# Kernel tuning notes

Hardware: AMD Instinct MI355X
Metric: run time of the kernel (lower is better)

## Reference

```python
import jax, jax.numpy as jnp
from jax import lax
import numpy as np

B, T, C = 2048, 512, 32  # batch, max_seq_len, num_tags


def setup_inputs() -> dict:
    key = jax.random.key(0)
    k1, k2, k3, k4 = jax.random.split(key, 4)
    logits = jax.random.normal(k1, (B, T, C), dtype=jnp.float32)
    sequence_length = jax.random.randint(k2, (B,), 1, T + 1, dtype=jnp.int32)
    labels = jax.random.randint(k3, (B, T), 0, C, dtype=jnp.int32)
    # learned CRF transition matrix (orthogonal init approximated by normal)
    transitions = jax.random.normal(k4, (C, C), dtype=jnp.float32)
    return dict(logits=logits, sequence_length=sequence_length,
                labels=labels, transitions=transitions)


def _viterbi_decode(logits, transitions, seq_len):
    """tfa_text.crf_decode: returns highest-scoring tag sequence [B, T] int32."""
    Bn, Tn, Cn = logits.shape
    identity_bp = jnp.arange(Cn, dtype=jnp.int32)[None, :]  # carries tag through padding

    def fwd(state, xs):  # state: [B, C] viterbi scores
        logit_t, t = xs
        scores = state[:, :, None] + transitions[None]       # [B, C_prev, C_cur]
        cand = logit_t + jnp.max(scores, axis=1)             # [B, C]
        bp = jnp.argmax(scores, axis=1).astype(jnp.int32)    # [B, C] best prev tag
        active = (t < seq_len)[:, None]
        return (jnp.where(active, cand, state),
                jnp.where(active, bp, identity_bp))

    xs = (jnp.swapaxes(logits[:, 1:], 0, 1), jnp.arange(1, Tn))
    final_state, bps = lax.scan(fwd, logits[:, 0], xs)       # bps: [T-1, B, C]
    last_tag = jnp.argmax(final_state, axis=-1).astype(jnp.int32)  # [B]

    def back(tag, bp):  # tag at t+1 -> tag at t
        prev = jnp.take_along_axis(bp, tag[:, None], axis=1)[:, 0]
        return prev, tag

    first_tag, later_tags = lax.scan(back, last_tag, bps, reverse=True)
    tags = jnp.concatenate([first_tag[None], later_tags], axis=0).T  # [B, T]
    valid = jnp.arange(Tn)[None, :] < seq_len[:, None]
    return jnp.where(valid, tags, 0)


def _crf_log_likelihood(logits, labels, transitions, seq_len):
    """tfa_text.crf_log_likelihood: per-example log-likelihood [B]."""
    Bn, Tn, Cn = logits.shape

    # --- log partition via forward algorithm ---
    def fwd(alpha, xs):
        logit_t, t = xs
        new = jax.nn.logsumexp(alpha[:, :, None] + transitions[None], axis=1) + logit_t
        active = (t < seq_len)[:, None]
        return jnp.where(active, new, alpha), None

    xs = (jnp.swapaxes(logits[:, 1:], 0, 1), jnp.arange(1, Tn))
    alpha, _ = lax.scan(fwd, logits[:, 0], xs)
    log_norm = jax.nn.logsumexp(alpha, axis=-1)  # [B]

    # --- score of gold label sequence ---
    pos = jnp.arange(Tn)
    mask = (pos[None, :] < seq_len[:, None]).astype(logits.dtype)          # [B, T]
    unary = jnp.sum(
        jnp.take_along_axis(logits, labels[..., None], axis=2)[..., 0] * mask,
        axis=1)
    pair_mask = (pos[None, :-1] < (seq_len - 1)[:, None]).astype(logits.dtype)
    binary = jnp.sum(transitions[labels[:, :-1], labels[:, 1:]] * pair_mask, axis=1)

    return unary + binary - log_norm


def reference(logits, sequence_length, labels, transitions):
    # training=True path: labels clamped to >= 0 (already non-negative here)
    labels = jnp.maximum(labels, 0)
    decode_tags = _viterbi_decode(logits, transitions, sequence_length)
    log_likelihood = _crf_log_likelihood(logits, labels, transitions, sequence_length)
    loss = jnp.mean(-log_likelihood)  # recorded via add_loss in the original
    return decode_tags, loss
```

## Files before the change

kernel.cpp:

```cpp
#include <hip/hip_runtime.h>
#include <math.h>

#define BB 2048
#define TT 512
#define CC 32

#if __has_builtin(__builtin_amdgcn_exp2f)
#define EXP2F __builtin_amdgcn_exp2f
#else
#define EXP2F exp2f
#endif
#if __has_builtin(__builtin_amdgcn_logf)
#define LOG2F __builtin_amdgcn_logf
#else
#define LOG2F log2f
#endif

#define LOG2E 1.4426950408889634f
#define LN2   0.6931471805599453f

__global__ void zero_loss_kernel(float* __restrict__ out) {
  if (threadIdx.x == 0) out[(size_t)BB * TT] = 0.0f;
}

__global__ void schedule_kernel(const int* __restrict__ seqlen,
                                int* __restrict__ perm,
                                float* __restrict__ out) {
  __shared__ int s[TT];
  __shared__ int off[TT];
  const int tid = threadIdx.x;
  if (tid == 0) out[(size_t)BB * TT] = 0.0f;
  s[tid] = 0;
  __syncthreads();
  for (int b = tid; b < BB; b += TT) atomicAdd(&s[seqlen[b] - 1], 1);
  __syncthreads();
  for (int d = 1; d < TT; d <<= 1) {
    int v = s[tid] + ((tid + d < TT) ? s[tid + d] : 0);
    __syncthreads();
    s[tid] = v;
    __syncthreads();
  }
  off[tid] = (tid + 1 < TT) ? s[tid + 1] : 0;
  __syncthreads();
  for (int b = tid; b < BB; b += TT) {
    int pos = atomicAdd(&off[seqlen[b] - 1], 1);
    perm[pos] = b;
  }
}

#define ROR(dst, src, K)                                                     \
  dst = __int_as_float(__builtin_amdgcn_update_dpp(                          \
      0, __float_as_int(src), 0x120 | (K), 0xF, 0xF, false));

__device__ __forceinline__ float xor16f(float x, int lane) {
#if __has_builtin(__builtin_amdgcn_permlane16_swap)
  auto r = __builtin_amdgcn_permlane16_swap(__float_as_uint(x),
                                            __float_as_uint(x), false, false);
  return __uint_as_float((lane & 16) ? r[0] : r[1]);
#else
  return __int_as_float(
      __builtin_amdgcn_ds_swizzle(__float_as_int(x), 0x401F));
#endif
}
__device__ __forceinline__ float xor32f(float x, int lane) {
#if __has_builtin(__builtin_amdgcn_permlane32_swap)
  auto r = __builtin_amdgcn_permlane32_swap(__float_as_uint(x),
                                            __float_as_uint(x), false, false);
  return __uint_as_float((lane & 32) ? r[0] : r[1]);
#else
  return __shfl_xor(x, 32);
#endif
}
__device__ __forceinline__ int xor32i(int x, int lane) {
#if __has_builtin(__builtin_amdgcn_permlane32_swap)
  auto r = __builtin_amdgcn_permlane32_swap((unsigned)x, (unsigned)x,
                                            false, false);
  return (int)((lane & 32) ? r[0] : r[1]);
#else
  return __shfl_xor(x, 32);
#endif
}

__global__ __launch_bounds__(128, 2) void crf_kernel(
    const float* __restrict__ logits,
    const int*   __restrict__ seqlen,
    const int*   __restrict__ labels,
    const float* __restrict__ trans,
    float*       __restrict__ out,
    const int*   __restrict__ perm)
{
  __shared__ __align__(16) unsigned char bp_s[(TT - 1) * CC];
  __shared__ __align__(16) unsigned gp_s[(TT / 4) * CC];
  __shared__ unsigned char tag_s[TT];

  const int lane = threadIdx.x & 63;
  const int wv   = threadIdx.x >> 6;
  const int k    = blockIdx.x;

  const int bs0 = perm ? perm[k] : k;
  const int bs1 = perm ? perm[BB - 1 - k] : -1;

  const int i  = lane & 15;
  const int c  = lane & 31;
  const int r  = (lane >> 4) & 1;
  const int pr = (lane < 32) ? r : 1 - r;

  if (wv == 0) {
    float tr2[16];
    int   pidx[16];
#pragma unroll
    for (int kk = 0; kk < 16; ++kk) {
      int p = pr * 16 + ((i - kk) & 15);
      pidx[kk] = p;
      tr2[kk] = trans[p * CC + c];
    }

    for (int sq = 0; sq < 2; ++sq) {
      const int b = sq ? bs1 : bs0;
      if (b < 0) break;
      const int len = seqlen[b];
      const float* lg = logits + (size_t)b * TT * CC;
      const size_t bT = (size_t)b * TT;
      const float* lgc = lg + c;

      float av = lg[c];

      auto vstep = [&](int t, float logit_c) -> int {
        float base = (lane < 32) ? av : xor16f(av, lane);
        float S[16];
        float x;
        S[0] = base + tr2[0];
        ROR(x, base, 1);  S[1]  = x + tr2[1];
        ROR(x, base, 2);  S[2]  = x + tr2[2];
        ROR(x, base, 3);  S[3]  = x + tr2[3];
        ROR(x, base, 4);  S[4]  = x + tr2[4];
        ROR(x, base, 5);  S[5]  = x + tr2[5];
        ROR(x, base, 6);  S[6]  = x + tr2[6];
        ROR(x, base, 7);  S[7]  = x + tr2[7];
        ROR(x, base, 8);  S[8]  = x + tr2[8];
        ROR(x, base, 9);  S[9]  = x + tr2[9];
        ROR(x, base, 10); S[10] = x + tr2[10];
        ROR(x, base, 11); S[11] = x + tr2[11];
        ROR(x, base, 12); S[12] = x + tr2[12];
        ROR(x, base, 13); S[13] = x + tr2[13];
        ROR(x, base, 14); S[14] = x + tr2[14];
        ROR(x, base, 15); S[15] = x + tr2[15];

        float a = fmaxf(fmaxf(S[0], S[1]), S[2]);
        float bq = fmaxf(fmaxf(S[3], S[4]), S[5]);
        float cq = fmaxf(fmaxf(S[6], S[7]), S[8]);
        float dq = fmaxf(fmaxf(S[9], S[10]), S[11]);
        float eq = fmaxf(fmaxf(S[12], S[13]), S[14]);
        float best = fmaxf(fmaxf(fmaxf(a, bq), fmaxf(cq, dq)),
                           fmaxf(eq, S[15]));

        int t8[16];
#pragma unroll
        for (int kk = 0; kk < 16; ++kk)
          t8[kk] = (S[kk] == best) ? pidx[kk] : 63;
        int ma = min(min(t8[0], t8[1]), t8[2]);
        int mb = min(min(t8[3], t8[4]), t8[5]);
        int mc = min(min(t8[6], t8[7]), t8[8]);
        int md = min(min(t8[9], t8[10]), t8[11]);
        int me = min(min(t8[12], t8[13]), t8[14]);
        int bi = min(min(min(ma, mb), min(mc, md)), min(me, t8[15]));

        float ov = xor32f(best, lane);
        int   oi = xor32i(bi, lane);
        bool take = (ov > best) || (ov == best && oi < bi);
        best = take ? ov : best;
        int bpi = take ? oi : bi;
        av = logit_c + best;

        if (lane < 32) bp_s[(t - 1) * CC + c] = (unsigned char)bpi;
        return bpi;
      };

      float Abk[8], Bbk[8];
      auto loadB = [&](float (&bk)[8], int t0) {
#pragma unroll
        for (int s = 0; s < 8; ++s) {
          int tt = t0 + s; tt = tt < len ? tt : len - 1;
          bk[s] = lgc[tt * CC];
        }
      };
      auto runB = [&](float (&bk)[8], int t0) {
        int h1 = 0, h2 = 0, h3 = 0;
#pragma unroll
        for (int s = 0; s < 8; ++s) {
          int tt = t0 + s;
          if (tt < len) {
            int bpi = vstep(tt, bk[s]);
            if ((tt & 3) == 0) {
              int m2 = __builtin_amdgcn_ds_bpermute(bpi << 2, h1);
              int m3 = __builtin_amdgcn_ds_bpermute(m2 << 2, h2);
              int m4 = __builtin_amdgcn_ds_bpermute(m3 << 2, h3);
              unsigned packed = (unsigned)bpi | ((unsigned)m2 << 8) |
                                ((unsigned)m3 << 16) | ((unsigned)m4 << 24);
              if (lane < 32) gp_s[((tt >> 2) - 1) * CC + c] = packed;
            }
            h3 = h2; h2 = h1; h1 = bpi;
          }
        }
      };
      loadB(Abk, 1);
      for (int t0 = 1; t0 < len; t0 += 16) {
        loadB(Bbk, t0 + 8);
        runB(Abk, t0);
        if (t0 + 8 < len) {
          loadB(Abk, t0 + 16);
          runB(Bbk, t0 + 8);
        }
      }

      float v = av; int idx = c;
#pragma unroll
      for (int d = 1; d < 32; d <<= 1) {
        float v2 = __shfl_xor(v, d, 32);
        int   i2 = __shfl_xor(idx, d, 32);
        if (v2 > v || (v2 == v && i2 < idx)) { v = v2; idx = i2; }
      }

      if (lane == 0) {
        int tag = idx;
        int t = len - 1;
        tag_s[t] = (unsigned char)tag;
        while (t > 0 && (t & 3) != 0) {
          tag = bp_s[(t - 1) * CC + tag];
          --t;
          tag_s[t] = (unsigned char)tag;
        }
        while (t >= 4) {
          unsigned u = gp_s[((t >> 2) - 1) * CC + tag];
          tag_s[t - 1] = (unsigned char)(u & 255);
          tag_s[t - 2] = (unsigned char)((u >> 8) & 255);
          tag_s[t - 3] = (unsigned char)((u >> 16) & 255);
          tag = (int)(u >> 24);
          tag_s[t - 4] = (unsigned char)tag;
          t -= 4;
        }
      }

#pragma unroll
      for (int j = 0; j < 8; ++j) {
        int tt = lane + 64 * j;
        float val = (tt < len) ? (float)tag_s[tt] : 0.0f;
        out[bT + tt] = val;
      }
    }

  } else {
    float E[16];
#pragma unroll
    for (int kk = 0; kk < 16; ++kk) {
      int p = pr * 16 + ((i - kk) & 15);
      E[kk] = EXP2F(trans[p * CC + c] * LOG2E);
    }

    float loss_acc = 0.0f;

    for (int sq = 0; sq < 2; ++sq) {
      const int b = sq ? bs1 : bs0;
      if (b < 0) break;
      const int len = seqlen[b];
      const float* lg = logits + (size_t)b * TT * CC;
      const int* lab = labels + (size_t)b * TT;
      const float* lgc = lg + c;

      float P   = EXP2F(lg[c] * LOG2E);
      float Acc = 0.0f;

      auto fstep = [&](float raw_logit) {
        float el = EXP2F(raw_logit * LOG2E);
        float base = (lane < 32) ? P : xor16f(P, lane);
        float x;
        float a0 = base * E[0];
        ROR(x, base, 1);  float a1 = x * E[1];
        ROR(x, base, 2);  float a2 = x * E[2];
        ROR(x, base, 3);  float a3 = x * E[3];
        ROR(x, base, 4);  a0 = fmaf(x, E[4],  a0);
        ROR(x, base, 5);  a1 = fmaf(x, E[5],  a1);
        ROR(x, base, 6);  a2 = fmaf(x, E[6],  a2);
        ROR(x, base, 7);  a3 = fmaf(x, E[7],  a3);
        ROR(x, base, 8);  a0 = fmaf(x, E[8],  a0);
        ROR(x, base, 9);  a1 = fmaf(x, E[9],  a1);
        ROR(x, base, 10); a2 = fmaf(x, E[10], a2);
        ROR(x, base, 11); a3 = fmaf(x, E[11], a3);
        ROR(x, base, 12); a0 = fmaf(x, E[12], a0);
        ROR(x, base, 13); a1 = fmaf(x, E[13], a1);
        ROR(x, base, 14); a2 = fmaf(x, E[14], a2);
        ROR(x, base, 15); a3 = fmaf(x, E[15], a3);
        float part = (a0 + a1) + (a2 + a3);
        float oth  = xor32f(part, lane);
        P = el * (part + oth);
      };

      auto renorm = [&]() {
        float m = P, y;
        ROR(y, m, 8); m = fmaxf(m, y);
        ROR(y, m, 4); m = fmaxf(m, y);
        ROR(y, m, 2); m = fmaxf(m, y);
        ROR(y, m, 1); m = fmaxf(m, y);
        m = fmaxf(m, xor16f(m, lane));
        int e = (int)(__float_as_uint(m) >> 23) - 127;
        P = ldexpf(P, -e);
        Acc += (float)e;
      };

      float Abk[8], Bbk[8];
      auto loadB = [&](float (&bk)[8], int t0) {
#pragma unroll
        for (int s = 0; s < 8; ++s) {
          int tt = t0 + s; tt = tt < len ? tt : len - 1;
          bk[s] = lgc[tt * CC];
        }
      };
      auto runB = [&](float (&bk)[8], int t0) {
#pragma unroll
        for (int s = 0; s < 8; ++s) {
          int tt = t0 + s;
          if (tt < len) {
            fstep(bk[s]);
            if ((tt & 3) == 0) renorm();
          }
        }
      };
      loadB(Abk, 1);
      for (int t0 = 1; t0 < len; t0 += 16) {
        loadB(Bbk, t0 + 8);
        runB(Abk, t0);
        if (t0 + 8 < len) {
          loadB(Abk, t0 + 16);
          runB(Bbk, t0 + 8);
        }
      }

      float uacc = 0.0f, bacc = 0.0f;
#pragma unroll
      for (int j = 0; j < 8; ++j) {
        int tt = lane + 64 * j;
        if (tt < len) {
          int lt = lab[tt];
          uacc += lg[tt * CC + lt];
          if (tt + 1 < len) {
            int ln = lab[tt + 1];
            bacc += trans[lt * CC + ln];
          }
        }
      }
#pragma unroll
      for (int d = 32; d >= 1; d >>= 1) {
        uacc += __shfl_xor(uacc, d);
        bacc += __shfl_xor(bacc, d);
      }

      float ss = P, y2;
      ROR(y2, ss, 8); ss += y2;
      ROR(y2, ss, 4); ss += y2;
      ROR(y2, ss, 2); ss += y2;
      ROR(y2, ss, 1); ss += y2;
      ss += xor16f(ss, lane);
      float log_norm = LN2 * (Acc + LOG2F(ss));

      loss_acc += (uacc + bacc - log_norm);
    }

    if (lane == 0) {
      atomicAdd(out + (size_t)BB * TT, loss_acc * (-1.0f / BB));
    }
  }
}

extern "C" void kernel_launch(void* const* d_in, const int* in_sizes, int n_in,
                              void* d_out, int out_size, void* d_ws, size_t ws_size,
                              hipStream_t stream) {
  const float* logits = (const float*)d_in[0];
  const int*   seqlen = (const int*)d_in[1];
  const int*   labels = (const int*)d_in[2];
  const float* trans  = (const float*)d_in[3];
  float* out = (float*)d_out;

  if (d_ws != nullptr && ws_size >= BB * sizeof(int)) {
    int* perm = (int*)d_ws;
    schedule_kernel<<<1, TT, 0, stream>>>(seqlen, perm, out);
    crf_kernel<<<dim3(BB / 2), dim3(128), 0, stream>>>(
        logits, seqlen, labels, trans, out, perm);
  } else {
    zero_loss_kernel<<<1, 64, 0, stream>>>(out);
    crf_kernel<<<dim3(BB), dim3(128), 0, stream>>>(
        logits, seqlen, labels, trans, out, nullptr);
  }
}
```

Measured before the change: 377.3 us.

## Process one sequence per block with interleaved length schedule and shrunk backpointer buffer

Each block now handles a single sequence instead of pairing a short and a long one, so the grid doubles to BB blocks. The schedule permutation is interleaved so blocks of similar length spread across CUs. The per-step backpointer shared buffer shrinks to a 4-step ring, which raises the occupancy hint to 4 blocks per CU. The loop is split into an unguarded full-chunk path and a guarded tail, and the max exchange is moved ahead of the argmax to shorten the critical path. The cost is losing the length balancing that pairing gave each block, plus relying on the scheduler for load balance.

```diff
diff --git a/kernel.cpp b/kernel.cpp
--- a/kernel.cpp
+++ b/kernel.cpp
@@ -43,8 +43,9 @@
   off[tid] = (tid + 1 < TT) ? s[tid + 1] : 0;
   __syncthreads();
   for (int b = tid; b < BB; b += TT) {
-    int pos = atomicAdd(&off[seqlen[b] - 1], 1);
-    perm[pos] = b;
+    int r = atomicAdd(&off[seqlen[b] - 1], 1);
+    int p = (r & 7) * 256 + (r >> 3);
+    perm[p] = b;
   }
 }
 
@@ -81,7 +82,7 @@
 #endif
 }
 
-__global__ __launch_bounds__(128, 2) void crf_kernel(
+__global__ __launch_bounds__(128, 4) void crf_kernel(
     const float* __restrict__ logits,
     const int*   __restrict__ seqlen,
     const int*   __restrict__ labels,
@@ -89,16 +90,18 @@
     float*       __restrict__ out,
     const int*   __restrict__ perm)
 {
-  __shared__ __align__(16) unsigned char bp_s[(TT - 1) * CC];
+  __shared__ __align__(16) unsigned char bp_s[4 * CC];
   __shared__ __align__(16) unsigned gp_s[(TT / 4) * CC];
   __shared__ unsigned char tag_s[TT];
 
   const int lane = threadIdx.x & 63;
   const int wv   = threadIdx.x >> 6;
-  const int k    = blockIdx.x;
-
-  const int bs0 = perm ? perm[k] : k;
-  const int bs1 = perm ? perm[BB - 1 - k] : -1;
+  const int b    = perm ? perm[blockIdx.x] : blockIdx.x;
+
+  const int len = seqlen[b];
+  const float* lg = logits + (size_t)b * TT * CC;
+  const size_t bT = (size_t)b * TT;
+  const float* lgc = lg + (lane & 31);
 
   const int i  = lane & 15;
   const int c  = lane & 31;
@@ -115,141 +118,152 @@
       tr2[kk] = trans[p * CC + c];
     }
 
-    for (int sq = 0; sq < 2; ++sq) {
-      const int b = sq ? bs1 : bs0;
-      if (b < 0) break;
-      const int len = seqlen[b];
-      const float* lg = logits + (size_t)b * TT * CC;
-      const size_t bT = (size_t)b * TT;
-      const float* lgc = lg + c;
-
-      float av = lg[c];
-
-      auto vstep = [&](int t, float logit_c) -> int {
-        float base = (lane < 32) ? av : xor16f(av, lane);
-        float S[16];
-        float x;
-        S[0] = base + tr2[0];
-        ROR(x, base, 1);  S[1]  = x + tr2[1];
-        ROR(x, base, 2);  S[2]  = x + tr2[2];
-        ROR(x, base, 3);  S[3]  = x + tr2[3];
-        ROR(x, base, 4);  S[4]  = x + tr2[4];
-        ROR(x, base, 5);  S[5]  = x + tr2[5];
-        ROR(x, base, 6);  S[6]  = x + tr2[6];
-        ROR(x, base, 7);  S[7]  = x + tr2[7];
-        ROR(x, base, 8);  S[8]  = x + tr2[8];
-        ROR(x, base, 9);  S[9]  = x + tr2[9];
-        ROR(x, base, 10); S[10] = x + tr2[10];
-        ROR(x, base, 11); S[11] = x + tr2[11];
-        ROR(x, base, 12); S[12] = x + tr2[12];
-        ROR(x, base, 13); S[13] = x + tr2[13];
-        ROR(x, base, 14); S[14] = x + tr2[14];
-        ROR(x, base, 15); S[15] = x + tr2[15];
-
-        float a = fmaxf(fmaxf(S[0], S[1]), S[2]);
-        float bq = fmaxf(fmaxf(S[3], S[4]), S[5]);
-        float cq = fmaxf(fmaxf(S[6], S[7]), S[8]);
-        float dq = fmaxf(fmaxf(S[9], S[10]), S[11]);
-        float eq = fmaxf(fmaxf(S[12], S[13]), S[14]);
-        float best = fmaxf(fmaxf(fmaxf(a, bq), fmaxf(cq, dq)),
-                           fmaxf(eq, S[15]));
-
-        int t8[16];
-#pragma unroll
-        for (int kk = 0; kk < 16; ++kk)
-          t8[kk] = (S[kk] == best) ? pidx[kk] : 63;
-        int ma = min(min(t8[0], t8[1]), t8[2]);
-        int mb = min(min(t8[3], t8[4]), t8[5]);
-        int mc = min(min(t8[6], t8[7]), t8[8]);
-        int md = min(min(t8[9], t8[10]), t8[11]);
-        int me = min(min(t8[12], t8[13]), t8[14]);
-        int bi = min(min(min(ma, mb), min(mc, md)), min(me, t8[15]));
-
-        float ov = xor32f(best, lane);
-        int   oi = xor32i(bi, lane);
-        bool take = (ov > best) || (ov == best && oi < bi);
-        best = take ? ov : best;
-        int bpi = take ? oi : bi;
-        av = logit_c + best;
-
-        if (lane < 32) bp_s[(t - 1) * CC + c] = (unsigned char)bpi;
-        return bpi;
-      };
-
-      float Abk[8], Bbk[8];
-      auto loadB = [&](float (&bk)[8], int t0) {
-#pragma unroll
-        for (int s = 0; s < 8; ++s) {
-          int tt = t0 + s; tt = tt < len ? tt : len - 1;
-          bk[s] = lgc[tt * CC];
+    float av = lg[c];
+
+    auto vstep = [&](int t, float logit_c) -> int {
+      float base = (lane < 32) ? av : xor16f(av, lane);
+      float S[16];
+      float x;
+      S[0] = base + tr2[0];
+      ROR(x, base, 1);  S[1]  = x + tr2[1];
+      ROR(x, base, 2);  S[2]  = x + tr2[2];
+      ROR(x, base, 3);  S[3]  = x + tr2[3];
+      ROR(x, base, 4);  S[4]  = x + tr2[4];
+      ROR(x, base, 5);  S[5]  = x + tr2[5];
+      ROR(x, base, 6);  S[6]  = x + tr2[6];
+      ROR(x, base, 7);  S[7]  = x + tr2[7];
+      ROR(x, base, 8);  S[8]  = x + tr2[8];
+      ROR(x, base, 9);  S[9]  = x + tr2[9];
+      ROR(x, base, 10); S[10] = x + tr2[10];
+      ROR(x, base, 11); S[11] = x + tr2[11];
+      ROR(x, base, 12); S[12] = x + tr2[12];
+      ROR(x, base, 13); S[13] = x + tr2[13];
+      ROR(x, base, 14); S[14] = x + tr2[14];
+      ROR(x, base, 15); S[15] = x + tr2[15];
+
+      float a = fmaxf(fmaxf(S[0], S[1]), S[2]);
+      float bq = fmaxf(fmaxf(S[3], S[4]), S[5]);
+      float cq = fmaxf(fmaxf(S[6], S[7]), S[8]);
+      float dq = fmaxf(fmaxf(S[9], S[10]), S[11]);
+      float eq = fmaxf(fmaxf(S[12], S[13]), S[14]);
+      float best = fmaxf(fmaxf(fmaxf(a, bq), fmaxf(cq, dq)),
+                         fmaxf(eq, S[15]));
+
+      float ov = xor32f(best, lane);
+      av = logit_c + fmaxf(best, ov);
+
+      int t8[16];
+#pragma unroll
+      for (int kk = 0; kk < 16; ++kk)
+        t8[kk] = (S[kk] == best) ? pidx[kk] : 63;
+      int ma = min(min(t8[0], t8[1]), t8[2]);
+      int mb = min(min(t8[3], t8[4]), t8[5]);
+      int mc = min(min(t8[6], t8[7]), t8[8]);
+      int md = min(min(t8[9], t8[10]), t8[11]);
+      int me = min(min(t8[12], t8[13]), t8[14]);
+      int bi = min(min(min(ma, mb), min(mc, md)), min(me, t8[15]));
+
+      int oi = xor32i(bi, lane);
+      bool take = (ov > best) || (ov == best && oi < bi);
+      int bpi = take ? oi : bi;
+
+      bp_s[((t - 1) & 3) * CC + c] = (unsigned char)bpi;
+      return bpi;
+    };
+
+    auto compose = [&](int tt, int b3, int b2, int b1, int b0) {
+      int m2 = __builtin_amdgcn_ds_bpermute(b3 << 2, b2);
+      int m3 = __builtin_amdgcn_ds_bpermute(m2 << 2, b1);
+      int m4 = __builtin_amdgcn_ds_bpermute(m3 << 2, b0);
+      unsigned packed = (unsigned)b3 | ((unsigned)m2 << 8) |
+                        ((unsigned)m3 << 16) | ((unsigned)m4 << 24);
+      gp_s[((tt >> 2) - 1) * CC + c] = packed;
+    };
+
+    float Abk[8], Bbk[8];
+    auto loadC = [&](float (&bk)[8], int t0) {
+#pragma unroll
+      for (int s = 0; s < 8; ++s) {
+        int tt = t0 + s; tt = tt < len ? tt : len - 1;
+        bk[s] = lgc[tt * CC];
+      }
+    };
+    auto runFull = [&](float (&bk)[8], int t0) {
+      int b0 = vstep(t0 + 0, bk[0]);
+      int b1 = vstep(t0 + 1, bk[1]);
+      int b2 = vstep(t0 + 2, bk[2]);
+      int b3 = vstep(t0 + 3, bk[3]);
+      compose(t0 + 3, b3, b2, b1, b0);
+      int b4 = vstep(t0 + 4, bk[4]);
+      int b5 = vstep(t0 + 5, bk[5]);
+      int b6 = vstep(t0 + 6, bk[6]);
+      int b7 = vstep(t0 + 7, bk[7]);
+      compose(t0 + 7, b7, b6, b5, b4);
+    };
+    auto runGuard = [&](float (&bk)[8], int t0) {
+      int h1 = 0, h2 = 0, h3 = 0;
+#pragma unroll
+      for (int s = 0; s < 8; ++s) {
+        int tt = t0 + s;
+        if (tt < len) {
+          int bpi = vstep(tt, bk[s]);
+          if ((tt & 3) == 0) compose(tt, bpi, h1, h2, h3);
+          h3 = h2; h2 = h1; h1 = bpi;
         }
-      };
-      auto runB = [&](float (&bk)[8], int t0) {
-        int h1 = 0, h2 = 0, h3 = 0;
-#pragma unroll
-        for (int s = 0; s < 8; ++s) {
-          int tt = t0 + s;
-          if (tt < len) {
-            int bpi = vstep(tt, bk[s]);
-            if ((tt & 3) == 0) {
-              int m2 = __builtin_amdgcn_ds_bpermute(bpi << 2, h1);
-              int m3 = __builtin_amdgcn_ds_bpermute(m2 << 2, h2);
-              int m4 = __builtin_amdgcn_ds_bpermute(m3 << 2, h3);
-              unsigned packed = (unsigned)bpi | ((unsigned)m2 << 8) |
-                                ((unsigned)m3 << 16) | ((unsigned)m4 << 24);
-              if (lane < 32) gp_s[((tt >> 2) - 1) * CC + c] = packed;
-            }
-            h3 = h2; h2 = h1; h1 = bpi;
-          }
-        }
-      };
-      loadB(Abk, 1);
-      for (int t0 = 1; t0 < len; t0 += 16) {
-        loadB(Bbk, t0 + 8);
-        runB(Abk, t0);
-        if (t0 + 8 < len) {
-          loadB(Abk, t0 + 16);
-          runB(Bbk, t0 + 8);
-        }
-      }
-
-      float v = av; int idx = c;
-#pragma unroll
-      for (int d = 1; d < 32; d <<= 1) {
-        float v2 = __shfl_xor(v, d, 32);
-        int   i2 = __shfl_xor(idx, d, 32);
-        if (v2 > v || (v2 == v && i2 < idx)) { v = v2; idx = i2; }
-      }
-
-      if (lane == 0) {
-        int tag = idx;
-        int t = len - 1;
+      }
+    };
+
+    loadC(Abk, 1);
+    int t0 = 1;
+    for (; t0 + 16 <= len; t0 += 16) {
+      loadC(Bbk, t0 + 8);
+      runFull(Abk, t0);
+      loadC(Abk, t0 + 16);
+      runFull(Bbk, t0 + 8);
+    }
+    if (t0 < len) {
+      loadC(Bbk, t0 + 8);
+      runGuard(Abk, t0);
+      if (t0 + 8 < len) runGuard(Bbk, t0 + 8);
+    }
+
+    float v = av; int idx = c;
+#pragma unroll
+    for (int d = 1; d < 32; d <<= 1) {
+      float v2 = __shfl_xor(v, d, 32);
+      int   i2 = __shfl_xor(idx, d, 32);
+      if (v2 > v || (v2 == v && i2 < idx)) { v = v2; idx = i2; }
+    }
+
+    if (lane == 0) {
+      int tag = idx;
+      int t = len - 1;
+      tag_s[t] = (unsigned char)tag;
+      while (t > 0 && (t & 3) != 0) {
+        tag = bp_s[((t - 1) & 3) * CC + tag];
+        --t;
         tag_s[t] = (unsigned char)tag;
-        while (t > 0 && (t & 3) != 0) {
-          tag = bp_s[(t - 1) * CC + tag];
-          --t;
-          tag_s[t] = (unsigned char)tag;
-        }
-        while (t >= 4) {
-          unsigned u = gp_s[((t >> 2) - 1) * CC + tag];
-          tag_s[t - 1] = (unsigned char)(u & 255);
-          tag_s[t - 2] = (unsigned char)((u >> 8) & 255);
-          tag_s[t - 3] = (unsigned char)((u >> 16) & 255);
-          tag = (int)(u >> 24);
-          tag_s[t - 4] = (unsigned char)tag;
-          t -= 4;
-        }
-      }
-
-#pragma unroll
-      for (int j = 0; j < 8; ++j) {
-        int tt = lane + 64 * j;
-        float val = (tt < len) ? (float)tag_s[tt] : 0.0f;
-        out[bT + tt] = val;
-      }
+      }
+      while (t >= 4) {
+        unsigned u = gp_s[((t >> 2) - 1) * CC + tag];
+        tag_s[t - 1] = (unsigned char)(u & 255);
+        tag_s[t - 2] = (unsigned char)((u >> 8) & 255);
+        tag_s[t - 3] = (unsigned char)((u >> 16) & 255);
+        tag = (int)(u >> 24);
+        tag_s[t - 4] = (unsigned char)tag;
+        t -= 4;
+      }
+    }
+
+#pragma unroll
+    for (int j = 0; j < 8; ++j) {
+      int tt = lane + 64 * j;
+      float val = (tt < len) ? (float)tag_s[tt] : 0.0f;
+      out[bT + tt] = val;
     }
 
   } else {
+    const int* lab = labels + (size_t)b * TT;
     float E[16];
 #pragma unroll
     for (int kk = 0; kk < 16; ++kk) {
@@ -257,116 +271,113 @@
       E[kk] = EXP2F(trans[p * CC + c] * LOG2E);
     }
 
-    float loss_acc = 0.0f;
-
-    for (int sq = 0; sq < 2; ++sq) {
-      const int b = sq ? bs1 : bs0;
-      if (b < 0) break;
-      const int len = seqlen[b];
-      const float* lg = logits + (size_t)b * TT * CC;
-      const int* lab = labels + (size_t)b * TT;
-      const float* lgc = lg + c;
-
-      float P   = EXP2F(lg[c] * LOG2E);
-      float Acc = 0.0f;
-
-      auto fstep = [&](float raw_logit) {
-        float el = EXP2F(raw_logit * LOG2E);
-        float base = (lane < 32) ? P : xor16f(P, lane);
-        float x;
-        float a0 = base * E[0];
-        ROR(x, base, 1);  float a1 = x * E[1];
-        ROR(x, base, 2);  float a2 = x * E[2];
-        ROR(x, base, 3);  float a3 = x * E[3];
-        ROR(x, base, 4);  a0 = fmaf(x, E[4],  a0);
-        ROR(x, base, 5);  a1 = fmaf(x, E[5],  a1);
-        ROR(x, base, 6);  a2 = fmaf(x, E[6],  a2);
-        ROR(x, base, 7);  a3 = fmaf(x, E[7],  a3);
-        ROR(x, base, 8);  a0 = fmaf(x, E[8],  a0);
-        ROR(x, base, 9);  a1 = fmaf(x, E[9],  a1);
-        ROR(x, base, 10); a2 = fmaf(x, E[10], a2);
-        ROR(x, base, 11); a3 = fmaf(x, E[11], a3);
-        ROR(x, base, 12); a0 = fmaf(x, E[12], a0);
-        ROR(x, base, 13); a1 = fmaf(x, E[13], a1);
-        ROR(x, base, 14); a2 = fmaf(x, E[14], a2);
-        ROR(x, base, 15); a3 = fmaf(x, E[15], a3);
-        float part = (a0 + a1) + (a2 + a3);
-        float oth  = xor32f(part, lane);
-        P = el * (part + oth);
-      };
-
-      auto renorm = [&]() {
-        float m = P, y;
-        ROR(y, m, 8); m = fmaxf(m, y);
-        ROR(y, m, 4); m = fmaxf(m, y);
-        ROR(y, m, 2); m = fmaxf(m, y);
-        ROR(y, m, 1); m = fmaxf(m, y);
-        m = fmaxf(m, xor16f(m, lane));
-        int e = (int)(__float_as_uint(m) >> 23) - 127;
-        P = ldexpf(P, -e);
-        Acc += (float)e;
-      };
-
-      float Abk[8], Bbk[8];
-      auto loadB = [&](float (&bk)[8], int t0) {
-#pragma unroll
-        for (int s = 0; s < 8; ++s) {
-          int tt = t0 + s; tt = tt < len ? tt : len - 1;
-          bk[s] = lgc[tt * CC];
+    float P   = EXP2F(lg[c] * LOG2E);
+    float Acc = 0.0f;
+
+    auto fstep = [&](float raw_logit) {
+      float el = EXP2F(raw_logit * LOG2E);
+      float base = (lane < 32) ? P : xor16f(P, lane);
+      float x;
+      float a0 = base * E[0];
+      ROR(x, base, 1);  float a1 = x * E[1];
+      ROR(x, base, 2);  float a2 = x * E[2];
+      ROR(x, base, 3);  float a3 = x * E[3];
+      ROR(x, base, 4);  a0 = fmaf(x, E[4],  a0);
+      ROR(x, base, 5);  a1 = fmaf(x, E[5],  a1);
+      ROR(x, base, 6);  a2 = fmaf(x, E[6],  a2);
+      ROR(x, base, 7);  a3 = fmaf(x, E[7],  a3);
+      ROR(x, base, 8);  a0 = fmaf(x, E[8],  a0);
+      ROR(x, base, 9);  a1 = fmaf(x, E[9],  a1);
+      ROR(x, base, 10); a2 = fmaf(x, E[10], a2);
+      ROR(x, base, 11); a3 = fmaf(x, E[11], a3);
+      ROR(x, base, 12); a0 = fmaf(x, E[12], a0);
+      ROR(x, base, 13); a1 = fmaf(x, E[13], a1);
+      ROR(x, base, 14); a2 = fmaf(x, E[14], a2);
+      ROR(x, base, 15); a3 = fmaf(x, E[15], a3);
+      float part = (a0 + a1) + (a2 + a3);
+      float oth  = xor32f(part, lane);
+      P = el * (part + oth);
+    };
+
+    auto renorm = [&]() {
+      float m = P, y;
+      ROR(y, m, 8); m = fmaxf(m, y);
+      ROR(y, m, 4); m = fmaxf(m, y);
+      ROR(y, m, 2); m = fmaxf(m, y);
+      ROR(y, m, 1); m = fmaxf(m, y);
+      m = fmaxf(m, xor16f(m, lane));
+      int e = (int)(__float_as_uint(m) >> 23) - 127;
+      P = ldexpf(P, -e);
+      Acc += (float)e;
+    };
+
+    float Abk[8], Bbk[8];
+    auto loadC = [&](float (&bk)[8], int t0) {
+#pragma unroll
+      for (int s = 0; s < 8; ++s) {
+        int tt = t0 + s; tt = tt < len ? tt : len - 1;
+        bk[s] = lgc[tt * CC];
+      }
+    };
+    auto runFull = [&](float (&bk)[8]) {
+      fstep(bk[0]); fstep(bk[1]); fstep(bk[2]); fstep(bk[3]); renorm();
+      fstep(bk[4]); fstep(bk[5]); fstep(bk[6]); fstep(bk[7]); renorm();
+    };
+    auto runGuard = [&](float (&bk)[8], int t0) {
+#pragma unroll
+      for (int s = 0; s < 8; ++s) {
+        int tt = t0 + s;
+        if (tt < len) {
+          fstep(bk[s]);
+          if ((tt & 3) == 0) renorm();
         }
-      };
-      auto runB = [&](float (&bk)[8], int t0) {
-#pragma unroll
-        for (int s = 0; s < 8; ++s) {
-          int tt = t0 + s;
-          if (tt < len) {
-            fstep(bk[s]);
-            if ((tt & 3) == 0) renorm();
-          }
+      }
+    };
+
+    loadC(Abk, 1);
+    int t0 = 1;
+    for (; t0 + 16 <= len; t0 += 16) {
+      loadC(Bbk, t0 + 8);
+      runFull(Abk);
+      loadC(Abk, t0 + 16);
+      runFull(Bbk);
+    }
+    if (t0 < len) {
+      loadC(Bbk, t0 + 8);
+      runGuard(Abk, t0);
+      if (t0 + 8 < len) runGuard(Bbk, t0 + 8);
+    }
+
+    float uacc = 0.0f, bacc = 0.0f;
+#pragma unroll
+    for (int j = 0; j < 8; ++j) {
+      int tt = lane + 64 * j;
+      if (tt < len) {
+        int lt = lab[tt];
+        uacc += lg[tt * CC + lt];
+        if (tt + 1 < len) {
+          int ln = lab[tt + 1];
+          bacc += trans[lt * CC + ln];
         }
-      };
-      loadB(Abk, 1);
-      for (int t0 = 1; t0 < len; t0 += 16) {
-        loadB(Bbk, t0 + 8);
-        runB(Abk, t0);
-        if (t0 + 8 < len) {
-          loadB(Abk, t0 + 16);
-          runB(Bbk, t0 + 8);
-        }
-      }
-
-      float uacc = 0.0f, bacc = 0.0f;
-#pragma unroll
-      for (int j = 0; j < 8; ++j) {
-        int tt = lane + 64 * j;
-        if (tt < len) {
-          int lt = lab[tt];
-          uacc += lg[tt * CC + lt];
-          if (tt + 1 < len) {
-            int ln = lab[tt + 1];
-            bacc += trans[lt * CC + ln];
-          }
-        }
-      }
-#pragma unroll
-      for (int d = 32; d >= 1; d >>= 1) {
-        uacc += __shfl_xor(uacc, d);
-        bacc += __shfl_xor(bacc, d);
-      }
-
-      float ss = P, y2;
-      ROR(y2, ss, 8); ss += y2;
-      ROR(y2, ss, 4); ss += y2;
-      ROR(y2, ss, 2); ss += y2;
-      ROR(y2, ss, 1); ss += y2;
-      ss += xor16f(ss, lane);
-      float log_norm = LN2 * (Acc + LOG2F(ss));
-
-      loss_acc += (uacc + bacc - log_norm);
-    }
+      }
+    }
+#pragma unroll
+    for (int d = 32; d >= 1; d >>= 1) {
+      uacc += __shfl_xor(uacc, d);
+      bacc += __shfl_xor(bacc, d);
+    }
+
+    float ss = P, y2;
+    ROR(y2, ss, 8); ss += y2;
+    ROR(y2, ss, 4); ss += y2;
+    ROR(y2, ss, 2); ss += y2;
+    ROR(y2, ss, 1); ss += y2;
+    ss += xor16f(ss, lane);
+    float log_norm = LN2 * (Acc + LOG2F(ss));
 
     if (lane == 0) {
-      atomicAdd(out + (size_t)BB * TT, loss_acc * (-1.0f / BB));
+      float ll = uacc + bacc - log_norm;
+      atomicAdd(out + (size_t)BB * TT, -ll * (1.0f / BB));
     }
   }
 }
@@ -383,7 +394,7 @@
   if (d_ws != nullptr && ws_size >= BB * sizeof(int)) {
     int* perm = (int*)d_ws;
     schedule_kernel<<<1, TT, 0, stream>>>(seqlen, perm, out);
-    crf_kernel<<<dim3(BB / 2), dim3(128), 0, stream>>>(
+    crf_kernel<<<dim3(BB), dim3(128), 0, stream>>>(
         logits, seqlen, labels, trans, out, perm);
   } else {
     zero_loss_kernel<<<1, 64, 0, stream>>>(out);
```

Result: slower. 477.4 us (+26.5%).
